# Optimization experiments

Hardware: AMD Instinct MI355X
Metric: run time of the kernel (lower is better)

## Reference

```python
import jax, jax.numpy as jnp
import numpy as np

B, INSIZE, H, OUT, STEPS = 8192, 256, 128, 1, 50


def setup_inputs() -> dict:
    key = jax.random.key(0)
    ks = jax.random.split(key, 16)
    s = 0.05
    inp = {
        "x": jax.random.normal(ks[0], (B, INSIZE), jnp.float32),
        # encoder MLP: 256 -> 128 -> 128 -> 128 (ReLU on hiddens, linear out)
        "ew0": jax.random.normal(ks[1], (INSIZE, 128), jnp.float32) * s,
        "eb0": jnp.zeros((128,), jnp.float32),
        "ew1": jax.random.normal(ks[2], (128, 128), jnp.float32) * s,
        "eb1": jnp.zeros((128,), jnp.float32),
        "ew2": jax.random.normal(ks[3], (128, H), jnp.float32) * s,
        "eb2": jnp.zeros((H,), jnp.float32),
        # GRU (input size OUT=1, hidden H=128), PyTorch layout [3H, in]/[3H, H]
        "w_ih": jax.random.normal(ks[4], (3 * H, OUT), jnp.float32) * s,
        "w_hh": jax.random.normal(ks[5], (3 * H, H), jnp.float32) * s,
        "b_ih": jnp.zeros((3 * H,), jnp.float32),
        "b_hh": jnp.zeros((3 * H,), jnp.float32),
        # decoder MLP: 128 -> 16 -> 1
        "dw0": jax.random.normal(ks[6], (H, 16), jnp.float32) * s,
        "db0": jnp.zeros((16,), jnp.float32),
        "dw1": jax.random.normal(ks[7], (16, OUT), jnp.float32) * s,
        "db1": jnp.zeros((OUT,), jnp.float32),
    }
    return inp


def _gru_cell(x_t, h, w_ih, w_hh, b_ih, b_hh):
    # PyTorch GRU cell: gates ordered [r, z, n]
    gx = x_t @ w_ih.T + b_ih  # [B, 3H]
    gh = h @ w_hh.T + b_hh    # [B, 3H]
    r = jax.nn.sigmoid(gx[:, :H] + gh[:, :H])
    z = jax.nn.sigmoid(gx[:, H:2 * H] + gh[:, H:2 * H])
    n = jnp.tanh(gx[:, 2 * H:] + r * gh[:, 2 * H:])
    return (1.0 - z) * n + z * h


def reference(x, ew0, eb0, ew1, eb1, ew2, eb2, w_ih, w_hh, b_ih, b_hh, dw0, db0, dw1, db1):
    # encoder MLP -> initial hidden state
    h = jax.nn.relu(x @ ew0 + eb0)
    h = jax.nn.relu(h @ ew1 + eb1)
    h = h @ ew2 + eb2  # [B, H]

    def step(carry, _):
        prev, hc = carry
        hn = _gru_cell(prev, hc, w_ih, w_hh, b_ih, b_hh)
        d = jax.nn.relu(hn @ dw0 + db0)
        out = d @ dw1 + db1  # [B, 1]
        return (out, hn), out

    prev0 = jnp.zeros((x.shape[0], OUT), x.dtype)
    _, outs = jax.lax.scan(step, (prev0, h), None, length=STEPS)  # [50, B, 1]
    outs = jnp.squeeze(outs, -1).T  # [B, 50]
    # torch: cat([zeros, out_0..out_49], dim=1)[..., :-1] -> [zeros, out_0..out_48]
    zeros = jnp.zeros((x.shape[0], 1), x.dtype)
    return jnp.concatenate([zeros, outs], axis=1)[:, :-1]
```

## Files before the change

kernel.cpp:

```cpp
#include <hip/hip_runtime.h>

#define NTH 512

typedef _Float16 half8 __attribute__((ext_vector_type(8)));
typedef _Float16 half4 __attribute__((ext_vector_type(4)));
typedef __attribute__((ext_vector_type(4))) float floatx4;

#define LOG2E 1.44269504088896340736f

template<int CTRL>
__device__ __forceinline__ float dpp_add(float v) {
    int o = __builtin_amdgcn_update_dpp(0, __float_as_int(v), CTRL, 0xF, 0xF, true);
    return v + __int_as_float(o);
}

#define MFMA16 __builtin_amdgcn_mfma_f32_16x16x32_f16

template<int KTILES, int CMASK, int ROWH>
__device__ __forceinline__ void enc_layer(const _Float16* __restrict__ src,
                                          const float* __restrict__ W,
                                          const float* __restrict__ bias,
                                          int jc, int quad, int l15,
                                          floatx4& acc) {
    const float bv = bias[jc];
    acc = (floatx4){bv, bv, bv, bv};
    #pragma unroll
    for (int kt = 0; kt < KTILES; kt++) {
        const int kb = kt * 32 + quad * 8;
        half8 hv;
        #pragma unroll
        for (int e = 0; e < 8; e++) hv[e] = (_Float16)W[(kb + e) * 128 + jc];
        const half8 av = *(const half8*)(src + l15 * ROWH +
                                         (((kt * 4 + quad) + l15) & CMASK) * 8);
        acc = MFMA16(av, hv, acc, 0, 0, 0);
    }
}

__device__ __forceinline__ void enc_store(_Float16* __restrict__ dst,
                                          const floatx4& acc,
                                          int jc, int quad, int l15, bool relu) {
    #pragma unroll
    for (int reg = 0; reg < 4; reg++) {
        const int row = quad * 4 + reg;
        float v = acc[reg];
        if (relu) v = fmaxf(v, 0.f);
        dst[row * 128 + ((((jc >> 3) + row) & 15) << 3) + (jc & 7)] = (_Float16)v;
    }
}

__global__ __launch_bounds__(NTH, 4)
void gru_fused_kernel(const float* __restrict__ x,
                      const float* __restrict__ ew0, const float* __restrict__ eb0,
                      const float* __restrict__ ew1, const float* __restrict__ eb1,
                      const float* __restrict__ ew2, const float* __restrict__ eb2,
                      const float* __restrict__ w_ih, const float* __restrict__ w_hh,
                      const float* __restrict__ b_ih, const float* __restrict__ b_hh,
                      const float* __restrict__ dw0, const float* __restrict__ db0,
                      const float* __restrict__ dw1, const float* __restrict__ db1,
                      float* __restrict__ out) {
    __shared__ __align__(16) _Float16 encx[16 * 256];
    __shared__ __align__(16) _Float16 h1b[16 * 128];
    __shared__ __align__(16) _Float16 h16[2 * 16 * 128];
    __shared__ float outb[16][52];

    const int tid  = threadIdx.x;
    const int b0   = blockIdx.x * 16;
    const int lane = tid & 63;
    const int w    = tid >> 6;
    const int quad = lane >> 4;
    const int l15  = lane & 15;
    const int jc   = w * 16 + l15;

    #pragma unroll
    for (int i = 0; i < 2; i++) {
        const int e = tid + i * NTH;
        const int row = e >> 6, c4 = e & 63;
        const float4 xv = *(const float4*)(x + (size_t)(b0 + row) * 256 + c4 * 4);
        half4 hv = {(_Float16)xv.x, (_Float16)xv.y, (_Float16)xv.z, (_Float16)xv.w};
        *(half4*)(encx + row * 256 + (((c4 >> 1) + row) & 31) * 8 + (c4 & 1) * 4) = hv;
    }
    __syncthreads();

    floatx4 ea;
    enc_layer<8, 31, 256>(encx, ew0, eb0, jc, quad, l15, ea);
    enc_store(h1b, ea, jc, quad, l15, true);
    __syncthreads();
    enc_layer<4, 15, 128>(h1b, ew1, eb1, jc, quad, l15, ea);
    enc_store(encx, ea, jc, quad, l15, true);
    __syncthreads();
    enc_layer<4, 15, 128>(encx, ew2, eb2, jc, quad, l15, ea);
    float hold[4];
    #pragma unroll
    for (int reg = 0; reg < 4; reg++) hold[reg] = ea[reg];
    enc_store(h16, ea, jc, quad, l15, false);
    if (tid < 16) outb[tid][0] = 0.f;

    half8 wb16[3][4];
    #pragma unroll
    for (int g = 0; g < 3; g++) {
        const float scale = (g == 2) ? 2.f * LOG2E : LOG2E;
        const float* wrow = w_hh + (g * 128 + jc) * 128;
        #pragma unroll
        for (int kt = 0; kt < 4; kt++) {
            const int kb = kt * 32 + quad * 8;
            half8 hv;
            #pragma unroll
            for (int e = 0; e < 8; e++) hv[e] = (_Float16)(wrow[kb + e] * scale);
            wb16[g][kt] = hv;
        }
    }
    half8 dw16[4];
    #pragma unroll
    for (int kt = 0; kt < 4; kt++) {
        half8 hv;
        #pragma unroll
        for (int e = 0; e < 8; e++)
            hv[e] = (_Float16)dw0[(kt * 32 + quad * 8 + e) * 16 + l15];
        dw16[kt] = hv;
    }
    const float wr   = w_ih[jc] * LOG2E;
    const float wz   = w_ih[128 + jc] * LOG2E;
    const float wn   = w_ih[256 + jc] * (2.f * LOG2E);
    const float c_r  = (b_ih[jc] + b_hh[jc]) * LOG2E;
    const float c_z  = (b_ih[128 + jc] + b_hh[128 + jc]) * LOG2E;
    const float c_n  = b_hh[256 + jc] * (2.f * LOG2E);
    const float bnih = b_ih[256 + jc] * (2.f * LOG2E);
    const float db0r = db0[l15];
    const float dw1r = dw1[l15];
    const float db1r = db1[0];
    __syncthreads();

    for (int t = 0; t <= 49; t++) {
        const int cur = t & 1, nxt = cur ^ 1;
        const _Float16* __restrict__ hc = h16 + cur * 2048;
        _Float16* __restrict__ hw = h16 + nxt * 2048;

        floatx4 dacc = (floatx4){db0r, db0r, db0r, db0r};
        floatx4 acc[3];
        acc[0] = (floatx4){c_r, c_r, c_r, c_r};
        acc[1] = (floatx4){c_z, c_z, c_z, c_z};
        acc[2] = (floatx4){c_n, c_n, c_n, c_n};
        #pragma unroll
        for (int kt = 0; kt < 4; kt++) {
            const half8 ahk = *(const half8*)(hc + l15 * 128 +
                                              (((kt * 4 + quad) + l15) & 15) * 8);
            dacc   = MFMA16(ahk, dw16[kt],    dacc,   0, 0, 0);
            acc[0] = MFMA16(ahk, wb16[0][kt], acc[0], 0, 0, 0);
            acc[1] = MFMA16(ahk, wb16[1][kt], acc[1], 0, 0, 0);
            acc[2] = MFMA16(ahk, wb16[2][kt], acc[2], 0, 0, 0);
        }

        float xp[4];
        #pragma unroll
        for (int reg = 0; reg < 4; reg++) {
            float v = fmaxf(dacc[reg], 0.f) * dw1r;
            v = dpp_add<0x140>(v);
            v = dpp_add<0x141>(v);
            v = dpp_add<0x4E>(v);
            v = dpp_add<0xB1>(v);
            xp[reg] = (t == 0) ? 0.f : (v + db1r);
        }
        if (t > 0 && w == 0 && l15 == 0) {
            #pragma unroll
            for (int reg = 0; reg < 4; reg++)
                outb[quad * 4 + reg][t] = xp[reg];
        }

        if (t < 49) {
            #pragma unroll
            for (int reg = 0; reg < 4; reg++) {
                const int row = quad * 4 + reg;
                const float xpv = xp[reg];
                const float hv0 = hold[reg];
                float gr = fmaf(xpv, wr, acc[0][reg]);
                float gz = fmaf(xpv, wz, acc[1][reg]);
                float Er = __builtin_amdgcn_exp2f(-gr);
                float rg = __builtin_amdgcn_rcpf(1.f + Er);
                float ys = fmaf(rg, acc[2][reg], fmaf(xpv, wn, bnih));
                float Ey = __builtin_amdgcn_exp2f(ys);
                float Ez = __builtin_amdgcn_exp2f(-gz);
                float u   = Ey + 1.f;
                float t1  = fmaf(Ez, Ey, -Ez);
                float num = fmaf(hv0, u, t1);
                float den = fmaf(Ez, u, u);
                const float hn = num * __builtin_amdgcn_rcpf(den);
                hold[reg] = hn;
                hw[row * 128 + ((((jc >> 3) + row) & 15) << 3) + (jc & 7)] =
                    (_Float16)hn;
            }
        }
        __syncthreads();
    }

    for (int e = tid; e < 16 * 50; e += NTH) {
        const int b = e / 50;
        const int tcol = e - b * 50;
        out[(size_t)b0 * 50 + e] = outb[b][tcol];
    }
}

extern "C" void kernel_launch(void* const* d_in, const int* in_sizes, int n_in,
                              void* d_out, int out_size, void* d_ws, size_t ws_size,
                              hipStream_t stream) {
    const float* x   = (const float*)d_in[0];
    const float* ew0 = (const float*)d_in[1];
    const float* eb0 = (const float*)d_in[2];
    const float* ew1 = (const float*)d_in[3];
    const float* eb1 = (const float*)d_in[4];
    const float* ew2 = (const float*)d_in[5];
    const float* eb2 = (const float*)d_in[6];
    const float* wih = (const float*)d_in[7];
    const float* whh = (const float*)d_in[8];
    const float* bih = (const float*)d_in[9];
    const float* bhh = (const float*)d_in[10];
    const float* dw0 = (const float*)d_in[11];
    const float* db0 = (const float*)d_in[12];
    const float* dw1 = (const float*)d_in[13];
    const float* db1 = (const float*)d_in[14];
    float* out = (float*)d_out;

    gru_fused_kernel<<<512, NTH, 0, stream>>>(
        x, ew0, eb0, ew1, eb1, ew2, eb2, wih, whh, bih, bhh,
        dw0, db0, dw1, db1, out);
}
```

Measured before the change: 193.6 us.

## Pin recurrent GRU weights in AGPRs and streamline the per-step loop

Inline asm forces the fp16 recurrent and decoder weight fragments into accumulation registers (AGPRs) and feeds them to the MFMA directly from there, which frees VGPRs under the 4-waves launch bound. LDS read and write offsets are hoisted out of the time loop, the W_hh loads are vectorized to float4, and s_setprio raises wave priority during the gate math. The risks are scheduling restrictions from the inline-asm MFMA and a possible mismatch between MFMA operand types and AGPR constraints.

```diff
diff --git a/kernel.cpp b/kernel.cpp
--- a/kernel.cpp
+++ b/kernel.cpp
@@ -15,6 +15,11 @@
 }
 
 #define MFMA16 __builtin_amdgcn_mfma_f32_16x16x32_f16
+
+__device__ __forceinline__ void mfma_ag(floatx4& c, half8 a, const half8& b) {
+    asm("v_mfma_f32_16x16x32_f16 %0, %1, %2, %0"
+        : "+v"(c) : "v"(a), "a"(b));
+}
 
 template<int KTILES, int CMASK, int ROWH>
 __device__ __forceinline__ void enc_layer(const _Float16* __restrict__ src,
@@ -103,9 +108,13 @@
         #pragma unroll
         for (int kt = 0; kt < 4; kt++) {
             const int kb = kt * 32 + quad * 8;
+            const float4 w0 = *(const float4*)(wrow + kb);
+            const float4 w1 = *(const float4*)(wrow + kb + 4);
             half8 hv;
-            #pragma unroll
-            for (int e = 0; e < 8; e++) hv[e] = (_Float16)(wrow[kb + e] * scale);
+            hv[0] = (_Float16)(w0.x * scale); hv[1] = (_Float16)(w0.y * scale);
+            hv[2] = (_Float16)(w0.z * scale); hv[3] = (_Float16)(w0.w * scale);
+            hv[4] = (_Float16)(w1.x * scale); hv[5] = (_Float16)(w1.y * scale);
+            hv[6] = (_Float16)(w1.z * scale); hv[7] = (_Float16)(w1.w * scale);
             wb16[g][kt] = hv;
         }
     }
@@ -118,6 +127,15 @@
             hv[e] = (_Float16)dw0[(kt * 32 + quad * 8 + e) * 16 + l15];
         dw16[kt] = hv;
     }
+    #pragma unroll
+    for (int g = 0; g < 3; g++)
+        #pragma unroll
+        for (int kt = 0; kt < 4; kt++)
+            asm volatile("" : "+a"(wb16[g][kt]));
+    #pragma unroll
+    for (int kt = 0; kt < 4; kt++)
+        asm volatile("" : "+a"(dw16[kt]));
+
     const float wr   = w_ih[jc] * LOG2E;
     const float wz   = w_ih[128 + jc] * LOG2E;
     const float wn   = w_ih[256 + jc] * (2.f * LOG2E);
@@ -128,6 +146,17 @@
     const float db0r = db0[l15];
     const float dw1r = dw1[l15];
     const float db1r = db1[0];
+
+    int rdo[4];
+    #pragma unroll
+    for (int kt = 0; kt < 4; kt++)
+        rdo[kt] = l15 * 128 + (((kt * 4 + quad) + l15) & 15) * 8;
+    int wro[4];
+    #pragma unroll
+    for (int reg = 0; reg < 4; reg++) {
+        const int row = quad * 4 + reg;
+        wro[reg] = row * 128 + ((((jc >> 3) + row) & 15) << 3) + (jc & 7);
+    }
     __syncthreads();
 
     for (int t = 0; t <= 49; t++) {
@@ -136,19 +165,19 @@
         _Float16* __restrict__ hw = h16 + nxt * 2048;
 
         floatx4 dacc = (floatx4){db0r, db0r, db0r, db0r};
-        floatx4 acc[3];
-        acc[0] = (floatx4){c_r, c_r, c_r, c_r};
-        acc[1] = (floatx4){c_z, c_z, c_z, c_z};
-        acc[2] = (floatx4){c_n, c_n, c_n, c_n};
+        floatx4 ar = (floatx4){c_r, c_r, c_r, c_r};
+        floatx4 az = (floatx4){c_z, c_z, c_z, c_z};
+        floatx4 an = (floatx4){c_n, c_n, c_n, c_n};
         #pragma unroll
         for (int kt = 0; kt < 4; kt++) {
-            const half8 ahk = *(const half8*)(hc + l15 * 128 +
-                                              (((kt * 4 + quad) + l15) & 15) * 8);
-            dacc   = MFMA16(ahk, dw16[kt],    dacc,   0, 0, 0);
-            acc[0] = MFMA16(ahk, wb16[0][kt], acc[0], 0, 0, 0);
-            acc[1] = MFMA16(ahk, wb16[1][kt], acc[1], 0, 0, 0);
-            acc[2] = MFMA16(ahk, wb16[2][kt], acc[2], 0, 0, 0);
-        }
+            const half8 ahk = *(const half8*)(hc + rdo[kt]);
+            mfma_ag(dacc, ahk, dw16[kt]);
+            mfma_ag(ar,   ahk, wb16[0][kt]);
+            mfma_ag(az,   ahk, wb16[1][kt]);
+            mfma_ag(an,   ahk, wb16[2][kt]);
+        }
+
+        __builtin_amdgcn_s_setprio(1);
 
         float xp[4];
         #pragma unroll
@@ -169,26 +198,25 @@
         if (t < 49) {
             #pragma unroll
             for (int reg = 0; reg < 4; reg++) {
-                const int row = quad * 4 + reg;
                 const float xpv = xp[reg];
                 const float hv0 = hold[reg];
-                float gr = fmaf(xpv, wr, acc[0][reg]);
-                float gz = fmaf(xpv, wz, acc[1][reg]);
+                float gr = fmaf(xpv, wr, ar[reg]);
+                float gz = fmaf(xpv, wz, az[reg]);
                 float Er = __builtin_amdgcn_exp2f(-gr);
+                float Ez = __builtin_amdgcn_exp2f(-gz);
                 float rg = __builtin_amdgcn_rcpf(1.f + Er);
-                float ys = fmaf(rg, acc[2][reg], fmaf(xpv, wn, bnih));
+                float ys = fmaf(rg, an[reg], fmaf(xpv, wn, bnih));
                 float Ey = __builtin_amdgcn_exp2f(ys);
-                float Ez = __builtin_amdgcn_exp2f(-gz);
                 float u   = Ey + 1.f;
                 float t1  = fmaf(Ez, Ey, -Ez);
                 float num = fmaf(hv0, u, t1);
                 float den = fmaf(Ez, u, u);
                 const float hn = num * __builtin_amdgcn_rcpf(den);
                 hold[reg] = hn;
-                hw[row * 128 + ((((jc >> 3) + row) & 15) << 3) + (jc & 7)] =
-                    (_Float16)hn;
+                hw[wro[reg]] = (_Float16)hn;
             }
         }
+        __builtin_amdgcn_s_setprio(0);
         __syncthreads();
     }
 
```

Measured after the change: 167.5 us. 1.16x faster.
